# Kernel tuning notes

Hardware: AMD Instinct MI355X
Metric: run time of the kernel (lower is better)

## Reference

```python
import jax, jax.numpy as jnp
import numpy as np

B, K, D, V = 4096, 128, 512, 128000


def setup_inputs() -> dict:
    key = jax.random.key(0)
    k1, k2, k3 = jax.random.split(key, 3)
    inp = jax.random.normal(k1, (B, D), dtype=jnp.float32)
    indices = jax.random.randint(k2, (B, K), 0, V, dtype=jnp.int64)
    # xavier_uniform: bound = sqrt(6/(fan_in+fan_out)) for weight [V, D]
    bound = float(np.sqrt(6.0 / (V + D)))
    weight = jax.random.uniform(k3, (V, D), dtype=jnp.float32, minval=-bound, maxval=bound)
    bias = jnp.zeros((V,), dtype=jnp.float32)
    return {"inp": inp, "indices": indices, "sparse": 1, "weight": weight, "bias": bias}


def reference(inp, indices, sparse, weight, bias):
    if sparse:
        # gather per-sample weight rows [B, K, D] and bias [B, K], then batched dot
        w = weight[indices]          # [B, K, D]
        b = bias[indices]            # [B, K]
        out = jnp.einsum('bkd,bd->bk', w, inp) + b
        return out
    else:
        return inp @ weight.T + bias
```

## Files before the change

### kernel.cpp

```cpp
#include <hip/hip_runtime.h>
#include <stdint.h>


constexpr int Kc = 128;
constexpr int Dc = 512;
constexpr int Vc = 128000;

__global__ __launch_bounds__(256) void SparseProjection_kernel(
    const float* __restrict__ inp,
    const int*   __restrict__ indices,
    const float* __restrict__ weight,
    const float* __restrict__ bias,
    float*       __restrict__ out)
{
    const int b    = blockIdx.x;
    const int tid  = threadIdx.x;
    const int lane = tid & 63;
    const int wave = tid >> 6;

    const float4* inp_row = (const float4*)(inp + (size_t)b * Dc);
    const float4 a0 = inp_row[lane];
    const float4 a1 = inp_row[64 + lane];

    const int* idx_base  = indices + (size_t)b * Kc;
    float*     out_base  = out     + (size_t)b * Kc;

    #pragma unroll 4
    for (int i = 0; i < 32; ++i) {
        const int k   = wave * 32 + i;
        const int idx = idx_base[k];
        const float4* wrow = (const float4*)(weight + (size_t)idx * Dc);

        const float4 w0 = wrow[lane];
        const float4 w1 = wrow[64 + lane];

        float s = a0.x * w0.x + a0.y * w0.y + a0.z * w0.z + a0.w * w0.w
                + a1.x * w1.x + a1.y * w1.y + a1.z * w1.z + a1.w * w1.w;

        #pragma unroll
        for (int off = 32; off > 0; off >>= 1)
            s += __shfl_xor(s, off, 64);

        if (lane == 0)
            out_base[k] = s + bias[idx];
    }
}


__global__ __launch_bounds__(256) void hist_kernel(
    const int* __restrict__ idx, unsigned int* __restrict__ counts, int n)
{
    int i      = blockIdx.x * blockDim.x + threadIdx.x;
    int stride = gridDim.x * blockDim.x;
    for (; i < n; i += stride)
        atomicAdd(&counts[idx[i]], 1u);
}

__global__ __launch_bounds__(256) void scan1_kernel(
    const unsigned int* __restrict__ counts, unsigned int* __restrict__ partials)
{
    __shared__ unsigned int sm[256];
    const int c = blockIdx.x;
    const int t = threadIdx.x;
    unsigned int a = counts[c * 512 + 2 * t] + counts[c * 512 + 2 * t + 1];
    sm[t] = a;
    __syncthreads();
    for (int off = 128; off > 0; off >>= 1) {
        if (t < off) sm[t] += sm[t + off];
        __syncthreads();
    }
    if (t == 0) partials[c] = sm[0];
}

__global__ __launch_bounds__(256) void scan2_kernel(
    unsigned int* __restrict__ partials, int nch)
{
    __shared__ unsigned int sm[256];
    const int t = threadIdx.x;
    unsigned int v = (t < nch) ? partials[t] : 0u;
    sm[t] = v;
    __syncthreads();
    for (int off = 1; off < 256; off <<= 1) {
        unsigned int add = (t >= off) ? sm[t - off] : 0u;
        __syncthreads();
        sm[t] += add;
        __syncthreads();
    }
    if (t < nch) partials[t] = sm[t] - v;
}

__global__ __launch_bounds__(256) void scan3_kernel(
    unsigned int* __restrict__ counts,
    const unsigned int* __restrict__ partials,
    unsigned int* __restrict__ starts,
    int n_total)
{
    __shared__ unsigned int sm[256];
    const int c    = blockIdx.x;
    const int t    = threadIdx.x;
    const int base = c * 512;
    unsigned int c0 = counts[base + 2 * t];
    unsigned int c1 = counts[base + 2 * t + 1];
    unsigned int pair = c0 + c1;
    sm[t] = pair;
    __syncthreads();
    for (int off = 1; off < 256; off <<= 1) {
        unsigned int add = (t >= off) ? sm[t - off] : 0u;
        __syncthreads();
        sm[t] += add;
        __syncthreads();
    }
    unsigned int excl = sm[t] - pair + partials[c];
    unsigned int s0 = excl;
    unsigned int s1 = excl + c0;
    starts[base + 2 * t]     = s0;
    starts[base + 2 * t + 1] = s1;
    counts[base + 2 * t]     = s0;
    counts[base + 2 * t + 1] = s1;
    if (c == 0 && t == 0) starts[Vc] = (unsigned int)n_total;
}

__global__ __launch_bounds__(256) void scatter_kernel(
    const int* __restrict__ idx, unsigned int* __restrict__ cursor,
    unsigned int* __restrict__ sorted, int n)
{
    int i      = blockIdx.x * blockDim.x + threadIdx.x;
    int stride = gridDim.x * blockDim.x;
    for (; i < n; i += stride) {
        int v = idx[i];
        unsigned int pos = atomicAdd(&cursor[v], 1u);
        sorted[pos] = (unsigned int)i;
    }
}

__global__ __launch_bounds__(256) void compute_sorted_kernel(
    const float* __restrict__ inp,
    const float* __restrict__ weight,
    const float* __restrict__ bias,
    const unsigned int* __restrict__ starts,
    const unsigned int* __restrict__ sorted,
    float* __restrict__ out)
{
    const int lane = threadIdx.x & 63;
    const int wave = threadIdx.x >> 6;
    const int v    = blockIdx.x * 4 + wave;

    const unsigned int s = starts[v];
    const unsigned int e = starts[v + 1];
    if (s == e) return;

    const float4* wrow = (const float4*)(weight + (size_t)v * Dc);
    const float4 w0 = wrow[lane];
    const float4 w1 = wrow[64 + lane];
    const float  bv = bias[v];

    for (unsigned int j = s; j < e; ++j) {
        const unsigned int bk = sorted[j];
        const float4* arow = (const float4*)(inp + (size_t)(bk >> 7) * Dc);
        const float4 a0 = arow[lane];
        const float4 a1 = arow[64 + lane];

        float sdot = a0.x * w0.x + a0.y * w0.y + a0.z * w0.z + a0.w * w0.w
                   + a1.x * w1.x + a1.y * w1.y + a1.z * w1.z + a1.w * w1.w;

        #pragma unroll
        for (int off = 32; off > 0; off >>= 1)
            sdot += __shfl_xor(sdot, off, 64);

        if (lane == 0)
            out[bk] = sdot + bv;
    }
}

extern "C" void kernel_launch(void* const* d_in, const int* in_sizes, int n_in,
                              void* d_out, int out_size, void* d_ws, size_t ws_size,
                              hipStream_t stream) {
    const float* inp     = (const float*)d_in[0];
    const int*   indices = (const int*)  d_in[1];
    const float* weight  = (const float*)d_in[3];
    const float* bias    = (const float*)d_in[4];
    float*       out     = (float*)d_out;

    const int B = in_sizes[0] / Dc;
    const int n = B * Kc;

    const size_t need_u32 = (size_t)2 * Vc + 64 + (size_t)n + 256;
    if (ws_size < need_u32 * sizeof(unsigned int)) {
        SparseProjection_kernel<<<B, 256, 0, stream>>>(inp, indices, weight, bias, out);
        return;
    }

    unsigned int* ws       = (unsigned int*)d_ws;
    unsigned int* counts   = ws;
    unsigned int* starts   = ws + Vc;
    unsigned int* sorted   = ws + 2 * Vc + 64;
    unsigned int* partials = sorted + n;

    hipMemsetAsync(counts, 0, (size_t)Vc * sizeof(unsigned int), stream);

    hist_kernel<<<2048, 256, 0, stream>>>(indices, counts, n);
    scan1_kernel<<<Vc / 512, 256, 0, stream>>>(counts, partials);
    scan2_kernel<<<1, 256, 0, stream>>>(partials, Vc / 512);
    scan3_kernel<<<Vc / 512, 256, 0, stream>>>(counts, partials, starts, n);
    scatter_kernel<<<2048, 256, 0, stream>>>(indices, counts, sorted, n);

    compute_sorted_kernel<<<Vc / 4, 256, 0, stream>>>(inp, weight, bias, starts, sorted, out);
}
```

Before: 472.9 us.

## Split D into four passes over sorted index list with partial sums and fixup

Replaces the per-vocab-row compute kernel with four passes that each handle a 128-wide slice of D over the sorted (sample, vocab) pairs. Partial dot products go to a workspace and a fixup kernel sums them, adds bias and scatters to the output. The intent is to shrink each pass's weight and input working set so it fits in cache, and to drop the per-row load imbalance from uneven bucket sizes. The hist and scatter kernels now read indices as int4. The cost is four extra partial-sum buffers, an extra kernel and more launches.

```diff
diff --git a/kernel.cpp b/kernel.cpp
--- a/kernel.cpp
+++ b/kernel.cpp
@@ -5,6 +5,8 @@
 constexpr int Kc = 128;
 constexpr int Dc = 512;
 constexpr int Vc = 128000;
+
+typedef float f4 __attribute__((ext_vector_type(4)));
 
 __global__ __launch_bounds__(256) void SparseProjection_kernel(
     const float* __restrict__ inp,
@@ -48,12 +50,17 @@
 
 
 __global__ __launch_bounds__(256) void hist_kernel(
-    const int* __restrict__ idx, unsigned int* __restrict__ counts, int n)
+    const int4* __restrict__ idx4, unsigned int* __restrict__ counts, int n4)
 {
     int i      = blockIdx.x * blockDim.x + threadIdx.x;
     int stride = gridDim.x * blockDim.x;
-    for (; i < n; i += stride)
-        atomicAdd(&counts[idx[i]], 1u);
+    for (; i < n4; i += stride) {
+        int4 v = idx4[i];
+        atomicAdd(&counts[v.x], 1u);
+        atomicAdd(&counts[v.y], 1u);
+        atomicAdd(&counts[v.z], 1u);
+        atomicAdd(&counts[v.w], 1u);
+    }
 }
 
 __global__ __launch_bounds__(256) void scan1_kernel(
@@ -91,9 +98,7 @@
 
 __global__ __launch_bounds__(256) void scan3_kernel(
     unsigned int* __restrict__ counts,
-    const unsigned int* __restrict__ partials,
-    unsigned int* __restrict__ starts,
-    int n_total)
+    const unsigned int* __restrict__ partials)
 {
     __shared__ unsigned int sm[256];
     const int c    = blockIdx.x;
@@ -111,64 +116,81 @@
         __syncthreads();
     }
     unsigned int excl = sm[t] - pair + partials[c];
-    unsigned int s0 = excl;
-    unsigned int s1 = excl + c0;
-    starts[base + 2 * t]     = s0;
-    starts[base + 2 * t + 1] = s1;
-    counts[base + 2 * t]     = s0;
-    counts[base + 2 * t + 1] = s1;
-    if (c == 0 && t == 0) starts[Vc] = (unsigned int)n_total;
+    counts[base + 2 * t]     = excl;
+    counts[base + 2 * t + 1] = excl + c0;
 }
 
 __global__ __launch_bounds__(256) void scatter_kernel(
-    const int* __restrict__ idx, unsigned int* __restrict__ cursor,
-    unsigned int* __restrict__ sorted, int n)
+    const int4* __restrict__ idx4, unsigned int* __restrict__ cursor,
+    unsigned int* __restrict__ sorted, unsigned int* __restrict__ sortedv, int n4)
 {
     int i      = blockIdx.x * blockDim.x + threadIdx.x;
     int stride = gridDim.x * blockDim.x;
-    for (; i < n; i += stride) {
-        int v = idx[i];
-        unsigned int pos = atomicAdd(&cursor[v], 1u);
-        sorted[pos] = (unsigned int)i;
-    }
-}
-
-__global__ __launch_bounds__(256) void compute_sorted_kernel(
+    for (; i < n4; i += stride) {
+        int4 v = idx4[i];
+        unsigned int base = 4u * (unsigned int)i;
+        unsigned int p;
+        p = atomicAdd(&cursor[v.x], 1u); sorted[p] = base + 0; sortedv[p] = (unsigned int)v.x;
+        p = atomicAdd(&cursor[v.y], 1u); sorted[p] = base + 1; sortedv[p] = (unsigned int)v.y;
+        p = atomicAdd(&cursor[v.z], 1u); sorted[p] = base + 2; sortedv[p] = (unsigned int)v.z;
+        p = atomicAdd(&cursor[v.w], 1u); sorted[p] = base + 3; sortedv[p] = (unsigned int)v.w;
+    }
+}
+
+__global__ __launch_bounds__(256) void compute_pass_kernel(
     const float* __restrict__ inp,
     const float* __restrict__ weight,
+    const unsigned int* __restrict__ sorted,
+    const unsigned int* __restrict__ sortedv,
+    float* __restrict__ out_part,
+    int dOff)
+{
+    const int lane = threadIdx.x & 63;
+    const int wid  = (blockIdx.x << 2) + (threadIdx.x >> 6);
+    const int j0   = wid << 6;
+    const int l32  = lane & 31;
+    const int half = lane >> 5;
+
+    const unsigned int s_bk = sorted[j0 + lane];
+    const unsigned int s_v  = sortedv[j0 + lane];
+
+    float* outp = out_part + j0;
+
+    #pragma unroll 4
+    for (int it = 0; it < 32; ++it) {
+        const int pslot = 2 * it + half;
+        const unsigned int bk = __shfl(s_bk, pslot, 64);
+        const unsigned int v  = __shfl(s_v,  pslot, 64);
+
+        const f4 w = __builtin_nontemporal_load(
+            (const f4*)(weight + (size_t)v * Dc + dOff) + l32);
+        const f4 a = *((const f4*)(inp + (size_t)(bk >> 7) * Dc + dOff) + l32);
+
+        float s = w.x * a.x + w.y * a.y + w.z * a.z + w.w * a.w;
+
+        s += __shfl_xor(s, 16, 64);
+        s += __shfl_xor(s,  8, 64);
+        s += __shfl_xor(s,  4, 64);
+        s += __shfl_xor(s,  2, 64);
+        s += __shfl_xor(s,  1, 64);
+
+        if (l32 == 0)
+            outp[pslot] = s;
+    }
+}
+
+__global__ __launch_bounds__(256) void fixup_kernel(
+    const unsigned int* __restrict__ sorted,
+    const unsigned int* __restrict__ sortedv,
+    const float* __restrict__ p0, const float* __restrict__ p1,
+    const float* __restrict__ p2, const float* __restrict__ p3,
     const float* __restrict__ bias,
-    const unsigned int* __restrict__ starts,
-    const unsigned int* __restrict__ sorted,
-    float* __restrict__ out)
-{
-    const int lane = threadIdx.x & 63;
-    const int wave = threadIdx.x >> 6;
-    const int v    = blockIdx.x * 4 + wave;
-
-    const unsigned int s = starts[v];
-    const unsigned int e = starts[v + 1];
-    if (s == e) return;
-
-    const float4* wrow = (const float4*)(weight + (size_t)v * Dc);
-    const float4 w0 = wrow[lane];
-    const float4 w1 = wrow[64 + lane];
-    const float  bv = bias[v];
-
-    for (unsigned int j = s; j < e; ++j) {
-        const unsigned int bk = sorted[j];
-        const float4* arow = (const float4*)(inp + (size_t)(bk >> 7) * Dc);
-        const float4 a0 = arow[lane];
-        const float4 a1 = arow[64 + lane];
-
-        float sdot = a0.x * w0.x + a0.y * w0.y + a0.z * w0.z + a0.w * w0.w
-                   + a1.x * w1.x + a1.y * w1.y + a1.z * w1.z + a1.w * w1.w;
-
-        #pragma unroll
-        for (int off = 32; off > 0; off >>= 1)
-            sdot += __shfl_xor(sdot, off, 64);
-
-        if (lane == 0)
-            out[bk] = sdot + bv;
+    float* __restrict__ out, int n)
+{
+    int j = blockIdx.x * blockDim.x + threadIdx.x;
+    if (j < n) {
+        float s = ((p0[j] + p1[j]) + (p2[j] + p3[j])) + bias[sortedv[j]];
+        out[sorted[j]] = s;
     }
 }
 
@@ -184,25 +206,37 @@
     const int B = in_sizes[0] / Dc;
     const int n = B * Kc;
 
-    const size_t need_u32 = (size_t)2 * Vc + 64 + (size_t)n + 256;
-    if (ws_size < need_u32 * sizeof(unsigned int)) {
+    const size_t need_u32 = (size_t)Vc + 256 + (size_t)2 * n + (size_t)4 * n;
+    if ((n & 255) != 0 || ws_size < need_u32 * sizeof(unsigned int)) {
         SparseProjection_kernel<<<B, 256, 0, stream>>>(inp, indices, weight, bias, out);
         return;
     }
 
     unsigned int* ws       = (unsigned int*)d_ws;
     unsigned int* counts   = ws;
-    unsigned int* starts   = ws + Vc;
-    unsigned int* sorted   = ws + 2 * Vc + 64;
-    unsigned int* partials = sorted + n;
+    unsigned int* partials = ws + Vc;
+    unsigned int* sorted   = ws + Vc + 256;
+    unsigned int* sortedv  = sorted + n;
+    float*        out_part = (float*)(sortedv + n);
+
+    const int n4 = n / 4;
 
     hipMemsetAsync(counts, 0, (size_t)Vc * sizeof(unsigned int), stream);
 
-    hist_kernel<<<2048, 256, 0, stream>>>(indices, counts, n);
+    hist_kernel<<<512, 256, 0, stream>>>((const int4*)indices, counts, n4);
     scan1_kernel<<<Vc / 512, 256, 0, stream>>>(counts, partials);
     scan2_kernel<<<1, 256, 0, stream>>>(partials, Vc / 512);
-    scan3_kernel<<<Vc / 512, 256, 0, stream>>>(counts, partials, starts, n);
-    scatter_kernel<<<2048, 256, 0, stream>>>(indices, counts, sorted, n);
-
-    compute_sorted_kernel<<<Vc / 4, 256, 0, stream>>>(inp, weight, bias, starts, sorted, out);
-}
+    scan3_kernel<<<Vc / 512, 256, 0, stream>>>(counts, partials);
+    scatter_kernel<<<512, 256, 0, stream>>>((const int4*)indices, counts,
+                                            sorted, sortedv, n4);
+
+    const int cgrid = n / 256;
+    for (int p = 0; p < 4; ++p) {
+        compute_pass_kernel<<<cgrid, 256, 0, stream>>>(
+            inp, weight, sorted, sortedv, out_part + (size_t)p * n, p * 128);
+    }
+
+    fixup_kernel<<<n / 256, 256, 0, stream>>>(sorted, sortedv,
+        out_part, out_part + n, out_part + 2 * (size_t)n, out_part + 3 * (size_t)n,
+        bias, out, n);
+}
```

Result: slower. 515.7 us (+9.0%).
